# Optimization experiments

Hardware: AMD Instinct MI355X
Metric: run time of the kernel (lower is better)

The kernel has to match this reference:

```python
import jax, jax.numpy as jnp
import numpy as np

B, NN, F, H = 8, 1024, 256, 8
D = F // H
SCALE = D ** -0.5


def setup_inputs() -> dict:
    key = jax.random.key(0)
    ks = jax.random.split(key, 12)
    s = 0.02
    inp = {
        'ndata': jax.random.normal(ks[0], (B, NN, F), jnp.float32),
        'N': NN,
        'attn_bias': jax.random.normal(ks[1], (B, NN, NN, H), jnp.float32),
        'attn_mask': jax.random.randint(ks[2], (B, NN, NN), 0, 2).astype(bool),
        'Wq': jax.random.normal(ks[3], (F, F), jnp.float32) * s,
        'bq': jnp.zeros((F,), jnp.float32),
        'Wk': jax.random.normal(ks[4], (F, F), jnp.float32) * s,
        'bk': jnp.zeros((F,), jnp.float32),
        'Wv': jax.random.normal(ks[5], (F, F), jnp.float32) * s,
        'bv': jnp.zeros((F,), jnp.float32),
        'Wo': jax.random.normal(ks[6], (F, F), jnp.float32) * s,
        'bo': jnp.zeros((F,), jnp.float32),
    }
    return inp


def reference(ndata, N, attn_bias, attn_mask, Wq, bq, Wk, bk, Wv, bv, Wo, bo):
    b, n, f = ndata.shape
    # QKV projections (torch nn.Linear: x @ W.T + b), split heads
    q = (ndata @ Wq.T + bq).reshape(b, n, H, D) * SCALE
    k = (ndata @ Wk.T + bk).reshape(b, n, H, D)
    v = (ndata @ Wv.T + bv).reshape(b, n, H, D)
    # scores: (b, q, k, h) matching torch layout after its transposes
    scores = jnp.einsum('bqhd,bkhd->bqkh', q, k)
    scores = scores + attn_bias  # additive bias
    # original code force-unmasks column 0 so every row has a valid entry
    mask = attn_mask.at[:, :, 0].set(False)
    scores = jnp.where(mask[..., None], -jnp.inf, scores)
    attn = jax.nn.softmax(scores, axis=2)  # softmax over keys
    out = jnp.einsum('bqkh,bkhd->bqhd', attn, v).reshape(b, n, f)
    return out @ Wo.T + bo
```

## Files before the change

kernel.cpp:

```cpp
#include <hip/hip_runtime.h>
#include <hip/hip_bf16.h>

typedef __attribute__((ext_vector_type(8))) short short8;
typedef __attribute__((ext_vector_type(4))) float f32x4;

#define MFMA16(a,b,c) __builtin_amdgcn_mfma_f32_16x16x32_bf16((a),(b),(c),0,0,0)

static __device__ __forceinline__ unsigned int f2bf(float f){
    unsigned int u = __float_as_uint(f);
    u += 0x7FFFu + ((u >> 16) & 1u);
    return u >> 16;
}

static __device__ __forceinline__ short8 pack8(float4 a, float4 b){
    short8 r;
    r[0]=(short)f2bf(a.x); r[1]=(short)f2bf(a.y);
    r[2]=(short)f2bf(a.z); r[3]=(short)f2bf(a.w);
    r[4]=(short)f2bf(b.x); r[5]=(short)f2bf(b.y);
    r[6]=(short)f2bf(b.z); r[7]=(short)f2bf(b.w);
    return r;
}

__global__ __launch_bounds__(256) void mask_prep_k(
    const unsigned int* __restrict__ m, unsigned int* __restrict__ bmout)
{
    __shared__ int any_hi;
    const int tid  = threadIdx.x;
    const int lane = tid & 63;
    const unsigned int gbase = blockIdx.x*256u + tid;
    if (tid == 0) any_hi = 0;

    unsigned int wv[8]; unsigned int acc = 0;
    #pragma unroll
    for (int it = 0; it < 8; ++it){
        wv[it] = m[it*262144u + gbase];
        acc |= wv[it];
    }
    __syncthreads();
    if (acc & 0xFFFFFF00u) atomicOr(&any_hi, 1);
    __syncthreads();

    if (any_hi == 0){
        for (int it = 0; it < 32; ++it){
            unsigned int idx = it*262144u + gbase;
            unsigned int v = m[idx];
            unsigned long long bal = __ballot(v != 0u);
            if (lane == 0)
                *(unsigned long long*)(bmout + (idx >> 5)) = bal;
        }
    } else {
        #pragma unroll
        for (int it = 0; it < 8; ++it){
            unsigned int idx = it*262144u + gbase;
            unsigned int v = wv[it];
            unsigned int nib = (v | (v>>7) | (v>>14) | (v>>21)) & 0xFu;
            unsigned int x = nib << ((lane & 7)*4);
            x |= (unsigned int)__shfl_xor((int)x, 1);
            x |= (unsigned int)__shfl_xor((int)x, 2);
            x |= (unsigned int)__shfl_xor((int)x, 4);
            if ((lane & 7) == 0)
                bmout[idx >> 3] = x;
        }
    }
}

__global__ __launch_bounds__(256) void qkv_proj_k(
    const float* __restrict__ nd,
    const float* __restrict__ Wqp, const float* __restrict__ bqp,
    const float* __restrict__ Wkp, const float* __restrict__ bkp,
    const float* __restrict__ Wvp, const float* __restrict__ bvp,
    unsigned short* __restrict__ qout, unsigned short* __restrict__ kout,
    unsigned short* __restrict__ vtout)
{
    __shared__ __align__(16) unsigned short xl[64*264];
    const int tid  = threadIdx.x;
    const int bi   = blockIdx.x;
    const int kind = bi >> 7;
    const int R0   = (bi & 127) * 64;
    const int b    = R0 >> 10;
    const int n0   = R0 & 1023;

    #pragma unroll
    for (int it = 0; it < 16; ++it){
        int f4 = it*256 + tid;
        int r = f4 >> 6, c4 = f4 & 63;
        float4 v = *(const float4*)(nd + (size_t)(R0+r)*256 + c4*4);
        unsigned int lo = f2bf(v.x) | (f2bf(v.y) << 16);
        unsigned int hi = f2bf(v.z) | (f2bf(v.w) << 16);
        *(uint2*)&xl[r*264 + c4*4] = make_uint2(lo, hi);
    }
    __syncthreads();

    const int lane = tid & 63;
    const int w  = tid >> 6;
    const int ln = lane & 15;
    const int g  = lane >> 4;
    const int ow = w * 64;

    f32x4 acc[4][4];
    #pragma unroll
    for (int a=0;a<4;++a){
        #pragma unroll
        for (int c=0;c<4;++c) acc[a][c] = (f32x4){0.f,0.f,0.f,0.f};
    }

    if (kind < 2){
        const float* W  = kind ? Wkp : Wqp;
        const float* bb = kind ? bkp : bqp;
        unsigned short* op = kind ? kout : qout;
        const float scl = kind ? 1.0f : 0.17677669529663687f;
        for (int kk = 0; kk < 8; ++kk){
            short8 wf[4], xf[4];
            #pragma unroll
            for (int ot=0; ot<4; ++ot){
                const float* wp = W + (size_t)(ow + ot*16 + ln)*256 + kk*32 + g*8;
                wf[ot] = pack8(*(const float4*)wp, *(const float4*)(wp+4));
            }
            #pragma unroll
            for (int nt=0; nt<4; ++nt)
                xf[nt] = *(const short8*)&xl[(nt*16+ln)*264 + kk*32 + g*8];
            #pragma unroll
            for (int ot=0; ot<4; ++ot){
                #pragma unroll
                for (int nt=0; nt<4; ++nt)
                    acc[ot][nt] = MFMA16(wf[ot], xf[nt], acc[ot][nt]);
            }
        }
        #pragma unroll
        for (int ot=0; ot<4; ++ot){
            int o0 = ow + ot*16 + g*4;
            int h = o0 >> 5, d0 = o0 & 31;
            float4 b4 = *(const float4*)(bb + o0);
            #pragma unroll
            for (int nt=0; nt<4; ++nt){
                int n = n0 + nt*16 + ln;
                unsigned int lo = f2bf((acc[ot][nt][0]+b4.x)*scl) | (f2bf((acc[ot][nt][1]+b4.y)*scl)<<16);
                unsigned int hi = f2bf((acc[ot][nt][2]+b4.z)*scl) | (f2bf((acc[ot][nt][3]+b4.w)*scl)<<16);
                *(uint2*)(op + ((size_t)(b*8+h)*1024 + n)*32 + d0) = make_uint2(lo,hi);
            }
        }
    } else {
        for (int kk = 0; kk < 8; ++kk){
            short8 wf[4], xf[4];
            #pragma unroll
            for (int ot=0; ot<4; ++ot){
                const float* wp = Wvp + (size_t)(ow + ot*16 + ln)*256 + kk*32 + g*8;
                wf[ot] = pack8(*(const float4*)wp, *(const float4*)(wp+4));
            }
            #pragma unroll
            for (int nt=0; nt<4; ++nt)
                xf[nt] = *(const short8*)&xl[(nt*16+ln)*264 + kk*32 + g*8];
            #pragma unroll
            for (int nt=0; nt<4; ++nt){
                #pragma unroll
                for (int ot=0; ot<4; ++ot)
                    acc[nt][ot] = MFMA16(xf[nt], wf[ot], acc[nt][ot]);
            }
        }
        #pragma unroll
        for (int nt=0; nt<4; ++nt){
            int nb = n0 + nt*16 + g*4;
            #pragma unroll
            for (int ot=0; ot<4; ++ot){
                int o = ow + ot*16 + ln;
                int h = o >> 5, d = o & 31;
                float bvv = bvp[o];
                unsigned int lo = f2bf(acc[nt][ot][0]+bvv) | (f2bf(acc[nt][ot][1]+bvv)<<16);
                unsigned int hi = f2bf(acc[nt][ot][2]+bvv) | (f2bf(acc[nt][ot][3]+bvv)<<16);
                *(uint2*)(vtout + ((size_t)(b*8+h)*32 + d)*1024 + nb) = make_uint2(lo,hi);
            }
        }
    }
}

__global__ __launch_bounds__(512, 4) void attn_k(
    const unsigned short* __restrict__ qbuf, const unsigned short* __restrict__ kbuf,
    const unsigned short* __restrict__ vtbuf, const float* __restrict__ bias,
    const unsigned int* __restrict__ bm, unsigned short* __restrict__ ab)
{
    __shared__ float bs[8192];
    const int tid  = threadIdx.x;
    const int bi   = blockIdx.x;
    const int b    = bi >> 6;
    const int q0   = (bi & 63) * 16;
    const int lane = tid & 63;
    const int w    = tid >> 6;
    const int ln   = lane & 15;
    const int g    = lane >> 4;

    const short8 qf = *(const short8*)(qbuf + ((size_t)(b*8+w)*1024 + q0 + ln)*32 + g*8);

    const int h2s  = lane & 1;
    const int keys = lane >> 1;
    const int ts   = keys >> 4;
    const int rs   = keys & 3;
    const int gs   = (keys >> 2) & 3;
    const int base0 = (128*ts + 32*rs + 16*h2s + gs) * 16;
    const int xrs   = (8*ts + 2*rs + h2s) & 15;
    const int qxa   = (2*w)     ^ xrs;
    const int qxb   = (2*w + 1) ^ xrs;

    const float* bp0 = bias + ((size_t)(b*1024 + q0 + 2*w)*1024)*8 + lane*4;
    const unsigned short* kp = kbuf  + ((size_t)(b*8+w)*1024 + ln)*32 + g*8;
    const unsigned short* vp = vtbuf + ((size_t)(b*8+w)*32   + ln)*1024 + g*8;
    const unsigned int*  bmp = bm + (size_t)(b*1024 + q0 + ln)*32;

    f32x4 acc0 = (f32x4){0.f,0.f,0.f,0.f};
    f32x4 acc1 = (f32x4){0.f,0.f,0.f,0.f};
    float lsum = 0.f;
    const f32x4 z4 = {0.f,0.f,0.f,0.f};

    float4 b00, b01, b10, b11;
    short8 kn0, kn1, kn2, kn3;
    unsigned int bm0, bm1;

#define LOAD_ALL(cc) do { int c_ = (cc); \
    b00 = *(const float4*)(bp0 + (size_t)c_*512); \
    b01 = *(const float4*)(bp0 + (size_t)c_*512 + 256); \
    b10 = *(const float4*)(bp0 + (size_t)c_*512 + 8192); \
    b11 = *(const float4*)(bp0 + (size_t)c_*512 + 8192 + 256); \
    kn0 = *(const short8*)(kp + c_*2048); \
    kn1 = *(const short8*)(kp + c_*2048 + 512); \
    kn2 = *(const short8*)(kp + c_*2048 + 1024); \
    kn3 = *(const short8*)(kp + c_*2048 + 1536); \
    bm0 = bmp[2*c_]; bm1 = bmp[2*c_+1]; } while(0)

#define CHUNK_HALF(K0, K1, BMW, BOFF, VOFF) do { \
    f32x4 s0 = MFMA16(K0, qf, z4); \
    f32x4 s1 = MFMA16(K1, qf, z4); \
    short8 vf0 = *(const short8*)(vp + (VOFF)); \
    short8 vf1 = *(const short8*)(vp + (VOFF) + 16*1024); \
    float pv[8]; \
    _Pragma("unroll") for (int t=0; t<2; ++t){ \
        _Pragma("unroll") for (int r=0; r<4; ++r){ \
            int keyl = t*16 + g*4 + r; \
            int bidx = (BOFF) + (t*128 + r*32 + w*4 + g)*16 + (ln ^ ((t*8 + r*2 + (w>>2)) & 15)); \
            float sv = (t ? s1[r] : s0[r]) + bs[bidx]; \
            sv = (((BMW) >> keyl) & 1u) ? -1e30f : sv; \
            float p = __expf(sv); \
            pv[t*4+r] = p; \
            lsum += p; \
        } \
    } \
    unsigned int A01 = f2bf(pv[0]) | (f2bf(pv[1])<<16); \
    unsigned int A23 = f2bf(pv[2]) | (f2bf(pv[3])<<16); \
    unsigned int B01 = f2bf(pv[4]) | (f2bf(pv[5])<<16); \
    unsigned int B23 = f2bf(pv[6]) | (f2bf(pv[7])<<16); \
    int s0l = (2*(g&1))*16 + ln; \
    int s1l = s0l + 16; \
    unsigned int a01  = (unsigned int)__shfl((int)A01, s0l); \
    unsigned int a23  = (unsigned int)__shfl((int)A23, s0l); \
    unsigned int c01  = (unsigned int)__shfl((int)B01, s0l); \
    unsigned int c23  = (unsigned int)__shfl((int)B23, s0l); \
    unsigned int a01b = (unsigned int)__shfl((int)A01, s1l); \
    unsigned int a23b = (unsigned int)__shfl((int)A23, s1l); \
    unsigned int c01b = (unsigned int)__shfl((int)B01, s1l); \
    unsigned int c23b = (unsigned int)__shfl((int)B23, s1l); \
    bool hi_ = (g >= 2); \
    int4 pw_ = make_int4((int)(hi_ ? c01  : a01 ), (int)(hi_ ? c23  : a23 ), \
                         (int)(hi_ ? c01b : a01b), (int)(hi_ ? c23b : a23b)); \
    short8 pf_ = *(short8*)&pw_; \
    acc0 = MFMA16(vf0, pf_, acc0); \
    acc1 = MFMA16(vf1, pf_, acc1); } while(0)

    LOAD_ALL(0);
    bm0 &= ~1u;

    #pragma unroll 1
    for (int cc = 0; cc < 16; ++cc){
        bs[base0       + qxa] = b00.x;  bs[base0 +  64 + qxa] = b00.y;
        bs[base0 + 128 + qxa] = b00.z;  bs[base0 + 192 + qxa] = b00.w;
        bs[base0       + qxb] = b10.x;  bs[base0 +  64 + qxb] = b10.y;
        bs[base0 + 128 + qxb] = b10.z;  bs[base0 + 192 + qxb] = b10.w;
        bs[4096 + base0       + qxa] = b01.x;  bs[4096 + base0 +  64 + qxa] = b01.y;
        bs[4096 + base0 + 128 + qxa] = b01.z;  bs[4096 + base0 + 192 + qxa] = b01.w;
        bs[4096 + base0       + qxb] = b11.x;  bs[4096 + base0 +  64 + qxb] = b11.y;
        bs[4096 + base0 + 128 + qxb] = b11.z;  bs[4096 + base0 + 192 + qxb] = b11.w;

        short8 ck0 = kn0, ck1 = kn1, ck2 = kn2, ck3 = kn3;
        unsigned int cb0 = bm0, cb1 = bm1;
        if (cc + 1 < 16) LOAD_ALL(cc + 1);
        __syncthreads();

        CHUNK_HALF(ck0, ck1, cb0, 0,    cc*64);
        CHUNK_HALF(ck2, ck3, cb1, 4096, cc*64 + 32);
        __syncthreads();
    }

    float ps = lsum;
    ps += __shfl_xor(ps, 16);
    ps += __shfl_xor(ps, 32);
    float inv = 1.0f / ps;
    {
        int n = q0 + ln;
        unsigned int lo0 = f2bf(acc0[0]*inv) | (f2bf(acc0[1]*inv)<<16);
        unsigned int hi0 = f2bf(acc0[2]*inv) | (f2bf(acc0[3]*inv)<<16);
        *(uint2*)(ab + ((size_t)(b*1024 + n))*256 + w*32 + g*4) = make_uint2(lo0,hi0);
        unsigned int lo1 = f2bf(acc1[0]*inv) | (f2bf(acc1[1]*inv)<<16);
        unsigned int hi1 = f2bf(acc1[2]*inv) | (f2bf(acc1[3]*inv)<<16);
        *(uint2*)(ab + ((size_t)(b*1024 + n))*256 + w*32 + 16 + g*4) = make_uint2(lo1,hi1);
    }
#undef LOAD_ALL
#undef CHUNK_HALF
}

__global__ __launch_bounds__(256) void oproj_k(
    const unsigned short* __restrict__ ab, const float* __restrict__ Wop,
    const float* __restrict__ bop, float* __restrict__ out)
{
    __shared__ __align__(16) unsigned short al[32*264];
    const int tid = threadIdx.x;
    const int R0 = blockIdx.x * 32;
    #pragma unroll
    for (int it=0; it<4; ++it){
        int f8 = it*256 + tid;
        int r = f8 >> 5, c8 = f8 & 31;
        *(short8*)&al[r*264 + c8*8] = *(const short8*)(ab + (size_t)(R0+r)*256 + c8*8);
    }
    __syncthreads();
    const int lane = tid & 63;
    const int w = tid >> 6, ln = lane & 15, g = lane >> 4;
    const int ow = w*64;
    f32x4 acc[4][2];
    #pragma unroll
    for (int a=0;a<4;++a){ acc[a][0]=(f32x4){0.f,0.f,0.f,0.f}; acc[a][1]=(f32x4){0.f,0.f,0.f,0.f}; }
    for (int kk=0;kk<8;++kk){
        short8 wf[4], xf[2];
        #pragma unroll
        for (int ot=0;ot<4;++ot){
            const float* wp = Wop + (size_t)(ow+ot*16+ln)*256 + kk*32 + g*8;
            wf[ot] = pack8(*(const float4*)wp, *(const float4*)(wp+4));
        }
        #pragma unroll
        for (int nt=0;nt<2;++nt)
            xf[nt] = *(const short8*)&al[(nt*16+ln)*264 + kk*32 + g*8];
        #pragma unroll
        for (int ot=0;ot<4;++ot){
            #pragma unroll
            for (int nt=0;nt<2;++nt)
                acc[ot][nt] = MFMA16(wf[ot], xf[nt], acc[ot][nt]);
        }
    }
    #pragma unroll
    for (int ot=0;ot<4;++ot){
        int o0 = ow + ot*16 + g*4;
        float4 b4 = *(const float4*)(bop + o0);
        #pragma unroll
        for (int nt=0;nt<2;++nt){
            int n = R0 + nt*16 + ln;
            float4 res;
            res.x = acc[ot][nt][0] + b4.x;
            res.y = acc[ot][nt][1] + b4.y;
            res.z = acc[ot][nt][2] + b4.z;
            res.w = acc[ot][nt][3] + b4.w;
            *(float4*)(out + (size_t)n*256 + o0) = res;
        }
    }
}

extern "C" void kernel_launch(void* const* d_in, const int* in_sizes, int n_in,
                              void* d_out, int out_size, void* d_ws, size_t ws_size,
                              hipStream_t stream)
{
    (void)in_sizes; (void)n_in; (void)out_size; (void)ws_size;
    const float* nd   = (const float*)d_in[0];
    const float* bias = (const float*)d_in[2];
    const int* mask   = (const int*)d_in[3];
    const float* Wq = (const float*)d_in[4];
    const float* bq = (const float*)d_in[5];
    const float* Wk = (const float*)d_in[6];
    const float* bk = (const float*)d_in[7];
    const float* Wv = (const float*)d_in[8];
    const float* bv = (const float*)d_in[9];
    const float* Wo = (const float*)d_in[10];
    const float* bo = (const float*)d_in[11];
    float* out = (float*)d_out;

    const size_t ELEMS = (size_t)8*8*1024*32;
    unsigned short* qb  = (unsigned short*)d_ws;
    unsigned short* kb  = qb  + ELEMS;
    unsigned short* vtb = kb  + ELEMS;
    unsigned short* ab  = vtb + ELEMS;
    unsigned int* bmw   = (unsigned int*)(ab + ELEMS);

    mask_prep_k<<<1024, 256, 0, stream>>>((const unsigned int*)mask, bmw);
    qkv_proj_k<<<384, 256, 0, stream>>>(nd, Wq, bq, Wk, bk, Wv, bv, qb, kb, vtb);
    attn_k<<<512, 512, 0, stream>>>(qb, kb, vtb, bias, bmw, ab);
    oproj_k<<<256, 256, 0, stream>>>(ab, Wo, bo, out);
}
```

Measured before the change: 143.6 us.

## Permute key rows so MFMA outputs map directly to PV operands, drop shuffles

Reorders the key rows fed to the QK MFMA so each lane's score outputs already sit in the layout the PV MFMA needs as its B operand. This removes the eight cross-lane shuffles and selects per chunk half. The bias staging in LDS is redone as a padded row-major layout, so each lane reads its eight bias values with two 16-byte LDS loads instead of eight scalar swizzled reads. Masked entries are now zeroed after the exp instead of being set to -1e30 before it. The padded buffer uses slightly more LDS and the stage-in stores may see different bank conflicts.

```diff
diff --git a/kernel.cpp b/kernel.cpp
--- a/kernel.cpp
+++ b/kernel.cpp
@@ -178,7 +178,7 @@
     const unsigned short* __restrict__ vtbuf, const float* __restrict__ bias,
     const unsigned int* __restrict__ bm, unsigned short* __restrict__ ab)
 {
-    __shared__ float bs[8192];
+    __shared__ __align__(16) float bs[8704];
     const int tid  = threadIdx.x;
     const int bi   = blockIdx.x;
     const int b    = bi >> 6;
@@ -190,75 +190,63 @@
 
     const short8 qf = *(const short8*)(qbuf + ((size_t)(b*8+w)*1024 + q0 + ln)*32 + g*8);
 
-    const int h2s  = lane & 1;
-    const int keys = lane >> 1;
-    const int ts   = keys >> 4;
-    const int rs   = keys & 3;
-    const int gs   = (keys >> 2) & 3;
-    const int base0 = (128*ts + 32*rs + 16*h2s + gs) * 16;
-    const int xrs   = (8*ts + 2*rs + h2s) & 15;
-    const int qxa   = (2*w)     ^ xrs;
-    const int qxb   = (2*w + 1) ^ xrs;
-
-    const float* bp0 = bias + ((size_t)(b*1024 + q0 + 2*w)*1024)*8 + lane*4;
-    const unsigned short* kp = kbuf  + ((size_t)(b*8+w)*1024 + ln)*32 + g*8;
+    const int kperm = ((ln >> 2) << 3) + (ln & 3);
+    const unsigned short* kp = kbuf  + ((size_t)(b*8+w)*1024 + kperm)*32 + g*8;
     const unsigned short* vp = vtbuf + ((size_t)(b*8+w)*32   + ln)*1024 + g*8;
     const unsigned int*  bmp = bm + (size_t)(b*1024 + q0 + ln)*32;
+
+    const int sq  = tid >> 5;
+    const float* bgp = bias + (size_t)(b*1024 + q0 + sq)*8192 + (tid & 31)*4;
+    const int hqb = (tid & 1)*4*1088 + sq*68;
+    const int kpw = (tid & 31) >> 1;
+    const int rb0 = w*1088 + ln*68 + 8*g;
 
     f32x4 acc0 = (f32x4){0.f,0.f,0.f,0.f};
     f32x4 acc1 = (f32x4){0.f,0.f,0.f,0.f};
     float lsum = 0.f;
     const f32x4 z4 = {0.f,0.f,0.f,0.f};
 
-    float4 b00, b01, b10, b11;
+    float4 br0, br1, br2, br3;
     short8 kn0, kn1, kn2, kn3;
     unsigned int bm0, bm1;
 
 #define LOAD_ALL(cc) do { int c_ = (cc); \
-    b00 = *(const float4*)(bp0 + (size_t)c_*512); \
-    b01 = *(const float4*)(bp0 + (size_t)c_*512 + 256); \
-    b10 = *(const float4*)(bp0 + (size_t)c_*512 + 8192); \
-    b11 = *(const float4*)(bp0 + (size_t)c_*512 + 8192 + 256); \
+    br0 = *(const float4*)(bgp + (size_t)c_*512); \
+    br1 = *(const float4*)(bgp + (size_t)c_*512 + 128); \
+    br2 = *(const float4*)(bgp + (size_t)c_*512 + 256); \
+    br3 = *(const float4*)(bgp + (size_t)c_*512 + 384); \
     kn0 = *(const short8*)(kp + c_*2048); \
-    kn1 = *(const short8*)(kp + c_*2048 + 512); \
+    kn1 = *(const short8*)(kp + c_*2048 + 128); \
     kn2 = *(const short8*)(kp + c_*2048 + 1024); \
-    kn3 = *(const short8*)(kp + c_*2048 + 1536); \
+    kn3 = *(const short8*)(kp + c_*2048 + 1152); \
     bm0 = bmp[2*c_]; bm1 = bmp[2*c_+1]; } while(0)
 
-#define CHUNK_HALF(K0, K1, BMW, BOFF, VOFF) do { \
-    f32x4 s0 = MFMA16(K0, qf, z4); \
-    f32x4 s1 = MFMA16(K1, qf, z4); \
+#define STAGE1(R, IT) do { int kw_ = (IT)*16 + kpw; \
+    bs[hqb        + kw_] = R.x; \
+    bs[hqb + 1088 + kw_] = R.y; \
+    bs[hqb + 2176 + kw_] = R.z; \
+    bs[hqb + 3264 + kw_] = R.w; } while(0)
+
+#define CHUNK_HALF(K0, K1, BMW, KH, VOFF) do { \
+    f32x4 s0 = MFMA16(K0, qf, z4);    \
+    f32x4 s1 = MFMA16(K1, qf, z4);    \
+    f32x4 blo = *(const f32x4*)&bs[rb0 + (KH)*32]; \
+    f32x4 bhi = *(const f32x4*)&bs[rb0 + (KH)*32 + 4]; \
     short8 vf0 = *(const short8*)(vp + (VOFF)); \
     short8 vf1 = *(const short8*)(vp + (VOFF) + 16*1024); \
-    float pv[8]; \
-    _Pragma("unroll") for (int t=0; t<2; ++t){ \
-        _Pragma("unroll") for (int r=0; r<4; ++r){ \
-            int keyl = t*16 + g*4 + r; \
-            int bidx = (BOFF) + (t*128 + r*32 + w*4 + g)*16 + (ln ^ ((t*8 + r*2 + (w>>2)) & 15)); \
-            float sv = (t ? s1[r] : s0[r]) + bs[bidx]; \
-            sv = (((BMW) >> keyl) & 1u) ? -1e30f : sv; \
-            float p = __expf(sv); \
-            pv[t*4+r] = p; \
-            lsum += p; \
-        } \
-    } \
-    unsigned int A01 = f2bf(pv[0]) | (f2bf(pv[1])<<16); \
-    unsigned int A23 = f2bf(pv[2]) | (f2bf(pv[3])<<16); \
-    unsigned int B01 = f2bf(pv[4]) | (f2bf(pv[5])<<16); \
-    unsigned int B23 = f2bf(pv[6]) | (f2bf(pv[7])<<16); \
-    int s0l = (2*(g&1))*16 + ln; \
-    int s1l = s0l + 16; \
-    unsigned int a01  = (unsigned int)__shfl((int)A01, s0l); \
-    unsigned int a23  = (unsigned int)__shfl((int)A23, s0l); \
-    unsigned int c01  = (unsigned int)__shfl((int)B01, s0l); \
-    unsigned int c23  = (unsigned int)__shfl((int)B23, s0l); \
-    unsigned int a01b = (unsigned int)__shfl((int)A01, s1l); \
-    unsigned int a23b = (unsigned int)__shfl((int)A23, s1l); \
-    unsigned int c01b = (unsigned int)__shfl((int)B01, s1l); \
-    unsigned int c23b = (unsigned int)__shfl((int)B23, s1l); \
-    bool hi_ = (g >= 2); \
-    int4 pw_ = make_int4((int)(hi_ ? c01  : a01 ), (int)(hi_ ? c23  : a23 ), \
-                         (int)(hi_ ? c01b : a01b), (int)(hi_ ? c23b : a23b)); \
+    unsigned int mb_ = (BMW) >> (g*8); \
+    float e0 = __expf(s0[0] + blo[0]); e0 = ((mb_>>0)&1u) ? 0.f : e0; \
+    float e1 = __expf(s0[1] + blo[1]); e1 = ((mb_>>1)&1u) ? 0.f : e1; \
+    float e2 = __expf(s0[2] + blo[2]); e2 = ((mb_>>2)&1u) ? 0.f : e2; \
+    float e3 = __expf(s0[3] + blo[3]); e3 = ((mb_>>3)&1u) ? 0.f : e3; \
+    float e4 = __expf(s1[0] + bhi[0]); e4 = ((mb_>>4)&1u) ? 0.f : e4; \
+    float e5 = __expf(s1[1] + bhi[1]); e5 = ((mb_>>5)&1u) ? 0.f : e5; \
+    float e6 = __expf(s1[2] + bhi[2]); e6 = ((mb_>>6)&1u) ? 0.f : e6; \
+    float e7 = __expf(s1[3] + bhi[3]); e7 = ((mb_>>7)&1u) ? 0.f : e7; \
+    lsum += ((e0+e1)+(e2+e3)) + ((e4+e5)+(e6+e7)); \
+    int4 pw_ = make_int4( \
+        (int)(f2bf(e0) | (f2bf(e1)<<16)), (int)(f2bf(e2) | (f2bf(e3)<<16)), \
+        (int)(f2bf(e4) | (f2bf(e5)<<16)), (int)(f2bf(e6) | (f2bf(e7)<<16))); \
     short8 pf_ = *(short8*)&pw_; \
     acc0 = MFMA16(vf0, pf_, acc0); \
     acc1 = MFMA16(vf1, pf_, acc1); } while(0)
@@ -268,22 +256,14 @@
 
     #pragma unroll 1
     for (int cc = 0; cc < 16; ++cc){
-        bs[base0       + qxa] = b00.x;  bs[base0 +  64 + qxa] = b00.y;
-        bs[base0 + 128 + qxa] = b00.z;  bs[base0 + 192 + qxa] = b00.w;
-        bs[base0       + qxb] = b10.x;  bs[base0 +  64 + qxb] = b10.y;
-        bs[base0 + 128 + qxb] = b10.z;  bs[base0 + 192 + qxb] = b10.w;
-        bs[4096 + base0       + qxa] = b01.x;  bs[4096 + base0 +  64 + qxa] = b01.y;
-        bs[4096 + base0 + 128 + qxa] = b01.z;  bs[4096 + base0 + 192 + qxa] = b01.w;
-        bs[4096 + base0       + qxb] = b11.x;  bs[4096 + base0 +  64 + qxb] = b11.y;
-        bs[4096 + base0 + 128 + qxb] = b11.z;  bs[4096 + base0 + 192 + qxb] = b11.w;
-
+        STAGE1(br0, 0); STAGE1(br1, 1); STAGE1(br2, 2); STAGE1(br3, 3);
         short8 ck0 = kn0, ck1 = kn1, ck2 = kn2, ck3 = kn3;
         unsigned int cb0 = bm0, cb1 = bm1;
         if (cc + 1 < 16) LOAD_ALL(cc + 1);
         __syncthreads();
 
-        CHUNK_HALF(ck0, ck1, cb0, 0,    cc*64);
-        CHUNK_HALF(ck2, ck3, cb1, 4096, cc*64 + 32);
+        CHUNK_HALF(ck0, ck1, cb0, 0, cc*64);
+        CHUNK_HALF(ck2, ck3, cb1, 1, cc*64 + 32);
         __syncthreads();
     }
 
@@ -301,6 +281,7 @@
         *(uint2*)(ab + ((size_t)(b*1024 + n))*256 + w*32 + 16 + g*4) = make_uint2(lo1,hi1);
     }
 #undef LOAD_ALL
+#undef STAGE1
 #undef CHUNK_HALF
 }
 
```

Measured after the change: 139.5 us. 1.03x faster.
